# Optimization experiments

Hardware: AMD Instinct MI355X
Metric: run time of the kernel (lower is better)

## Reference

```python
import jax, jax.numpy as jnp
import numpy as np

BATCH, SEQ, FEAT, NUM_BINS = 64, 1024, 512, 32


def setup_inputs() -> dict:
    key = jax.random.key(0)
    k1, k2 = jax.random.split(key)
    features = jax.random.normal(k1, (BATCH, SEQ, FEAT), dtype=jnp.float32)
    # buffer: randn(input_dim, num_bins) / sqrt(input_dim)
    random_projection = jax.random.normal(k2, (FEAT, NUM_BINS), dtype=jnp.float32) / np.sqrt(FEAT)
    return {"features": features, "random_projection": random_projection}


def reference(features, random_projection):
    batch, seq, feat = features.shape
    x = features.reshape(-1, feat)  # [N, feat]
    N = x.shape[0]

    # RunningMeanStd.update from fresh state (mean=0, var=1, count=1e-4)
    eps_count = 1e-4
    batch_mean = x.mean(axis=0)
    batch_var = jnp.var(x, axis=0, ddof=1)  # torch.var is unbiased by default
    tot = eps_count + N
    delta = batch_mean  # - 0
    mean = delta * N / tot
    M2 = 1.0 * eps_count + batch_var * N + (delta ** 2) * eps_count * N / tot
    var = M2 / tot
    sigma = jnp.sqrt(var + 1e-8)

    normalized = (x - mean) / sigma
    projected = normalized @ random_projection  # [N, num_bins]
    bits = (projected > 0).astype(jnp.int64)
    pow2 = jnp.left_shift(jnp.int64(1), jnp.arange(NUM_BINS, dtype=jnp.int64))
    keys = (bits * pow2).sum(axis=-1)  # [N], values < 2^32

    # env_indices=None path: env = arange(N) % batch
    env = jnp.arange(N, dtype=jnp.int64) % batch
    combined = jnp.left_shift(env, 32) | keys  # unique (env, key) id

    # running occurrence count of each (env, key) in sample order i=0..N-1
    order = jnp.argsort(combined, stable=True)  # stable: preserves sample order within group
    s = combined[order]
    idx = jnp.arange(N, dtype=jnp.int64)
    is_start = jnp.concatenate([jnp.ones((1,), bool), s[1:] != s[:-1]])
    seg_start = jax.lax.cummax(jnp.where(is_start, idx, 0))
    occ = idx - seg_start + 1  # 1-based occurrence within group
    counts = jnp.zeros((N,), jnp.int64).at[order].set(occ)

    rewards = 1.0 / jnp.sqrt(counts.astype(features.dtype))
    return rewards.reshape(batch, seq, 1)
```

## Files before the change

kernel.cpp:

```cpp
#include <hip/hip_runtime.h>

using u16 = unsigned short;
using u64 = unsigned long long;

constexpr int BATCH = 64, SEQ = 1024, FEAT = 512, NBINS = 32;
constexpr int N = BATCH * SEQ;
constexpr int TAB = 131072;
constexpr unsigned TABMASK = TAB - 1;
constexpr u64 EMPTY = ~0ull;
constexpr double FXSCALE = 67108864.0;
constexpr int NSHADOW = 64;


constexpr size_t OFF_KEYS = 0;
constexpr size_t OFF_HEAD = 1048576;
constexpr size_t OFF_CNT = 1572864;
constexpr size_t OFF_SHAD = 2097152;
constexpr size_t OFF_QD = 2621440;
constexpr size_t OFF_CD = 2752512;
constexpr size_t OFF_QF = 2752768;
constexpr size_t OFF_CF = 2818304;
constexpr size_t OFF_SLOT = 2818432;
constexpr size_t OFF_NEXT = 3080576;

__global__ __launch_bounds__(256, 4) void colstats_kernel(
    const float4* __restrict__ xv,
    u64* __restrict__ shad) {
  const int t = threadIdx.x;
  const int L = blockIdx.x * 256 + t;
  double s0 = 0, s1 = 0, s2 = 0, s3 = 0, q0 = 0, q1 = 0, q2 = 0, q3 = 0;
  for (int mm = 0; mm < 32; mm += 8) {
    float4 v[8];
#pragma unroll
    for (int u = 0; u < 8; u++) v[u] = xv[L + (mm + u) * 262144];
#pragma unroll
    for (int u = 0; u < 8; u++) {
      double a = (double)v[u].x, b = (double)v[u].y;
      double c = (double)v[u].z, d = (double)v[u].w;
      s0 += a; s1 += b; s2 += c; s3 += d;
      q0 += a * a; q1 += b * b; q2 += c * c; q3 += d * d;
    }
  }
  __shared__ double red[256 * 8];
  red[t * 8 + 0] = s0; red[t * 8 + 1] = s1; red[t * 8 + 2] = s2; red[t * 8 + 3] = s3;
  red[t * 8 + 4] = q0; red[t * 8 + 5] = q1; red[t * 8 + 6] = q2; red[t * 8 + 7] = q3;
  __syncthreads();
  if (t < 128) {
    double v[8];
#pragma unroll
    for (int u = 0; u < 8; u++) v[u] = red[t * 8 + u] + red[(t + 128) * 8 + u];
    const int c0 = 4 * t;
    u64* sh = shad + (size_t)(blockIdx.x & (NSHADOW - 1)) * 1024;
#pragma unroll
    for (int u = 0; u < 4; u++) {
      long long a = (long long)llrint(v[u] * FXSCALE);
      long long b = (long long)llrint(v[4 + u] * FXSCALE);
      atomicAdd(&sh[c0 + u], (u64)a);
      atomicAdd(&sh[512 + c0 + u], (u64)b);
    }
  }
}

__global__ __launch_bounds__(512) void finalize_kernel(
    const float* __restrict__ P,
    const u64* __restrict__ shad,
    double* __restrict__ Qd, float* __restrict__ Qf,
    double* __restrict__ cd, float* __restrict__ cf) {
  __shared__ double meanArr[FEAT];
  __shared__ double invArr[FEAT];
  __shared__ double part[16][NBINS];
  const int t = threadIdx.x;
  long long isum = 0, isumsq = 0;
  for (int sh = 0; sh < NSHADOW; sh++) {
    isum += (long long)shad[sh * 1024 + t];
    isumsq += (long long)shad[sh * 1024 + 512 + t];
  }
  const double Nd = (double)N;
  const double tot = 1e-4 + Nd;
  double s = (double)isum * (1.0 / FXSCALE);
  double ss = (double)isumsq * (1.0 / FXSCALE);
  double bm = s / Nd;
  double bv = (ss - s * s / Nd) / (Nd - 1.0);
  double mean = bm * Nd / tot;
  double M2 = 1e-4 + bv * Nd + bm * bm * 1e-4 * Nd / tot;
  double var = M2 / tot;
  double inv = 1.0 / sqrt(var + 1e-8);
  meanArr[t] = mean;
  invArr[t] = inv;
#pragma unroll
  for (int j = 0; j < NBINS; j++) {
    double qd = (double)P[t * NBINS + j] * inv;
    Qd[t * NBINS + j] = qd;
    Qf[t * NBINS + j] = (float)qd;
  }
  __syncthreads();
  {
    const int j = t & 31, g = t >> 5;
    double p = 0.0;
    for (int f = g * 32; f < g * 32 + 32; f++) {
      double qd = (double)P[f * NBINS + j] * invArr[f];
      p += meanArr[f] * qd;
    }
    part[g][j] = p;
  }
  __syncthreads();
  if (t < NBINS) {
    double c = 0.0;
    for (int g = 0; g < 16; g++) c += part[g][t];
    cd[t] = c;
    cf[t] = (float)c;
  }
}

constexpr float TAU = 2.5e-3f;
__global__ __launch_bounds__(256) void project_kernel(
    const float4* __restrict__ xv, const float* __restrict__ feat,
    const float4* __restrict__ Qf4, const float* __restrict__ cf,
    const double* __restrict__ Qd, const double* __restrict__ cd,
    u64* __restrict__ keys_tab, int* __restrict__ head,
    unsigned* __restrict__ cnt, int* __restrict__ slot, int* __restrict__ nxt) {
  __shared__ __align__(16) float xt[64 * 132];
  __shared__ __align__(16) float qt[128 * 32];
  __shared__ unsigned keyParts[64];
  const int t = threadIdx.x;
  const int rowBase = blockIdx.x * 64;
  const int lane = t & 63;
  const int wid = t >> 6;
  const int j0 = __builtin_amdgcn_readfirstlane(wid * 8);
  if (t < 64) keyParts[t] = 0u;
  float4* qt4 = (float4*)qt;

  float acc[8] = {0, 0, 0, 0, 0, 0, 0, 0};
  for (int ch = 0; ch < 4; ch++) {
    __syncthreads();
#pragma unroll
    for (int k = 0; k < 8; k++) {
      int vi = t + k * 256;
      int r = vi >> 5, fv = vi & 31;
      float4 v = xv[(size_t)(rowBase + r) * 128 + ch * 32 + fv];
      *((float4*)&xt[r * 132 + fv * 4]) = v;
    }
#pragma unroll
    for (int k = 0; k < 4; k++) {
      int qi = t + k * 256;
      qt4[qi] = Qf4[ch * 1024 + qi];
    }
    __syncthreads();
    const float4* xrow = (const float4*)&xt[lane * 132];
#pragma unroll 4
    for (int g = 0; g < 32; g++) {
      float4 x4 = xrow[g];
      float xs[4] = {x4.x, x4.y, x4.z, x4.w};
#pragma unroll
      for (int ff = 0; ff < 4; ff++) {
        const int fl = 4 * g + ff;
        float4 qlo = qt4[(fl * 32 + j0) >> 2];
        float4 qhi = qt4[(fl * 32 + j0 + 4) >> 2];
        float x = xs[ff];
        acc[0] = fmaf(x, qlo.x, acc[0]);
        acc[1] = fmaf(x, qlo.y, acc[1]);
        acc[2] = fmaf(x, qlo.z, acc[2]);
        acc[3] = fmaf(x, qlo.w, acc[3]);
        acc[4] = fmaf(x, qhi.x, acc[4]);
        acc[5] = fmaf(x, qhi.y, acc[5]);
        acc[6] = fmaf(x, qhi.z, acc[6]);
        acc[7] = fmaf(x, qhi.w, acc[7]);
      }
    }
  }
  unsigned part = 0;
  float m[8];
#pragma unroll
  for (int j = 0; j < 8; j++) {
    m[j] = acc[j] - cf[j0 + j];
    if (m[j] > 0.0f) part |= (1u << (j0 + j));
  }
  for (int j = 0; j < 8; j++) {
    u64 mask = __ballot(fabsf(m[j]) < TAU);
    const int jj = j0 + j;
    while (mask) {
      const int L = (int)__builtin_ctzll(mask);
      mask &= mask - 1;
      const float* xr = feat + (size_t)(rowBase + L) * FEAT + lane * 8;
      const double* qp = Qd + (size_t)(lane * 8) * NBINS + jj;
      double p = 0.0;
#pragma unroll
      for (int u = 0; u < 8; u++)
        p = fma((double)xr[u], qp[u * NBINS], p);
#pragma unroll
      for (int off = 32; off > 0; off >>= 1) p += __shfl_xor(p, off, 64);
      const bool bit = p > cd[jj];
      if (lane == L) {
        if (bit) part |= (1u << jj);
        else part &= ~(1u << jj);
      }
    }
  }
  atomicOr(&keyParts[lane], part);
  __syncthreads();
  if (t < 64) {
    const int i = rowBase + t;
    unsigned key = keyParts[t];
    u64 combined = (u64)key;
    unsigned idx = (unsigned)((combined * 0x9E3779B97F4A7C15ull) >> 47) & TABMASK;
    for (;;) {
      u64 prev = atomicCAS(&keys_tab[idx], EMPTY, combined);
      if (prev == EMPTY || prev == combined) break;
      idx = (idx + 1) & TABMASK;
    }
    slot[i] = (int)idx;
    atomicAdd(&cnt[idx], 1u);
    nxt[i] = atomicExch(&head[idx], i);
  }
}

__global__ __launch_bounds__(256) void count_kernel(
    const int* __restrict__ slot, const int* __restrict__ nxt,
    const int* __restrict__ head, const unsigned* __restrict__ cnt,
    float* __restrict__ out) {
  const int i = blockIdx.x * 256 + threadIdx.x;
  const int sl = slot[i];
  const unsigned c = cnt[sl];
  float r = 1.0f;
  if (c > 1u) {
    int j = head[sl];
    int occ = 1;
    while (j >= 0) {
      occ += (j < i) ? 1 : 0;
      j = nxt[j];
    }
    r = 1.0f / sqrtf((float)occ);
  }
  out[i] = r;
}

extern "C" void kernel_launch(void* const* d_in, const int* in_sizes, int n_in,
                              void* d_out, int out_size, void* d_ws, size_t ws_size,
                              hipStream_t stream) {
  const float4* xv = (const float4*)d_in[0];
  const float* feat = (const float*)d_in[0];
  const float* proj = (const float*)d_in[1];
  float* out = (float*)d_out;
  char* ws = (char*)d_ws;

  u64* keys_tab = (u64*)(ws + OFF_KEYS);
  int* head = (int*)(ws + OFF_HEAD);
  unsigned* cnt = (unsigned*)(ws + OFF_CNT);
  u64* shad = (u64*)(ws + OFF_SHAD);
  double* Qd = (double*)(ws + OFF_QD);
  double* cd = (double*)(ws + OFF_CD);
  float* Qf = (float*)(ws + OFF_QF);
  float* cf = (float*)(ws + OFF_CF);
  int* slot = (int*)(ws + OFF_SLOT);
  int* nxt = (int*)(ws + OFF_NEXT);

  hipMemsetAsync(ws + OFF_KEYS, 0xFF, OFF_CNT - OFF_KEYS, stream);
  hipMemsetAsync(ws + OFF_CNT, 0x00, OFF_QD - OFF_CNT, stream);

  colstats_kernel<<<1024, 256, 0, stream>>>(xv, shad);
  finalize_kernel<<<1, 512, 0, stream>>>(proj, shad, Qd, Qf, cd, cf);
  project_kernel<<<N / 64, 256, 0, stream>>>(xv, feat, (const float4*)Qf, cf, Qd, cd,
                                             keys_tab, head, cnt, slot, nxt);
  count_kernel<<<N / 256, 256, 0, stream>>>(slot, nxt, head, cnt, out);
}
```

Measured before the change: 290.6 us.

## Compute projection with split-bf16 MFMA instead of scalar FP32 FMAs

Replaces the FP32 FMA projection loop with MFMA 16x16x32 bf16 instructions. Inputs and the scaled projection matrix are split into bf16 high and low parts, and three products (hh, lh, hl) approximate FP32 accuracy. The projection matrix is pre-laid out in fragment order in finalize, and x tiles are converted and stored in swizzled LDS. The near-zero fallback to an exact FP64 recheck is kept, but the band may now trigger more often because the split-bf16 result has larger error.

```diff
diff --git a/kernel.cpp b/kernel.cpp
--- a/kernel.cpp
+++ b/kernel.cpp
@@ -2,6 +2,9 @@
 
 using u16 = unsigned short;
 using u64 = unsigned long long;
+typedef short s16x8 __attribute__((ext_vector_type(8)));
+typedef unsigned short u16x4 __attribute__((ext_vector_type(4)));
+typedef float f32x4 __attribute__((ext_vector_type(4)));
 
 constexpr int BATCH = 64, SEQ = 1024, FEAT = 512, NBINS = 32;
 constexpr int N = BATCH * SEQ;
@@ -18,14 +21,22 @@
 constexpr size_t OFF_SHAD = 2097152;
 constexpr size_t OFF_QD = 2621440;
 constexpr size_t OFF_CD = 2752512;
-constexpr size_t OFF_QF = 2752768;
 constexpr size_t OFF_CF = 2818304;
 constexpr size_t OFF_SLOT = 2818432;
 constexpr size_t OFF_NEXT = 3080576;
+constexpr size_t OFF_QFRAG = 3342720;
+
+__device__ inline u16 f2bf(float f) {
+  unsigned u = __builtin_bit_cast(unsigned, f);
+  u += 0x7FFFu + ((u >> 16) & 1u);
+  return (u16)(u >> 16);
+}
+__device__ inline float bf2f(u16 h) {
+  return __builtin_bit_cast(float, (unsigned)h << 16);
+}
 
 __global__ __launch_bounds__(256, 4) void colstats_kernel(
-    const float4* __restrict__ xv,
-    u64* __restrict__ shad) {
+    const float4* __restrict__ xv, u64* __restrict__ shad) {
   const int t = threadIdx.x;
   const int L = blockIdx.x * 256 + t;
   double s0 = 0, s1 = 0, s2 = 0, s3 = 0, q0 = 0, q1 = 0, q2 = 0, q3 = 0;
@@ -64,7 +75,7 @@
 __global__ __launch_bounds__(512) void finalize_kernel(
     const float* __restrict__ P,
     const u64* __restrict__ shad,
-    double* __restrict__ Qd, float* __restrict__ Qf,
+    double* __restrict__ Qd, u16* __restrict__ qfrag,
     double* __restrict__ cd, float* __restrict__ cf) {
   __shared__ double meanArr[FEAT];
   __shared__ double invArr[FEAT];
@@ -87,11 +98,19 @@
   double inv = 1.0 / sqrt(var + 1e-8);
   meanArr[t] = mean;
   invArr[t] = inv;
+  const int ch = t >> 7, ks = (t >> 5) & 3, kg = (t >> 3) & 3, jlo = t & 7;
 #pragma unroll
   for (int j = 0; j < NBINS; j++) {
     double qd = (double)P[t * NBINS + j] * inv;
     Qd[t * NBINS + j] = qd;
-    Qf[t * NBINS + j] = (float)qd;
+    const u16 qh = f2bf((float)qd);
+    const u16 ql = f2bf((float)(qd - (double)bf2f(qh)));
+    const int lane = (j & 15) | (kg << 4);
+    const int bt = j >> 4;
+    const size_t base =
+        (size_t)(((((ch * 4 + ks) * 2 + bt) * 2) * 64 + lane) * 8 + jlo);
+    qfrag[base] = qh;
+    qfrag[base + 512] = ql;
   }
   __syncthreads();
   {
@@ -113,90 +132,109 @@
 }
 
 constexpr float TAU = 2.5e-3f;
-__global__ __launch_bounds__(256) void project_kernel(
+__global__ __launch_bounds__(256, 3) void project_kernel(
     const float4* __restrict__ xv, const float* __restrict__ feat,
-    const float4* __restrict__ Qf4, const float* __restrict__ cf,
+    const u16* __restrict__ qfrag, const float* __restrict__ cf,
     const double* __restrict__ Qd, const double* __restrict__ cd,
     u64* __restrict__ keys_tab, int* __restrict__ head,
     unsigned* __restrict__ cnt, int* __restrict__ slot, int* __restrict__ nxt) {
-  __shared__ __align__(16) float xt[64 * 132];
-  __shared__ __align__(16) float qt[128 * 32];
+  __shared__ __align__(16) u16 xh_lds[8192];
+  __shared__ __align__(16) u16 xl_lds[8192];
   __shared__ unsigned keyParts[64];
   const int t = threadIdx.x;
   const int rowBase = blockIdx.x * 64;
   const int lane = t & 63;
-  const int wid = t >> 6;
-  const int j0 = __builtin_amdgcn_readfirstlane(wid * 8);
+  const int w = t >> 6;
   if (t < 64) keyParts[t] = 0u;
-  float4* qt4 = (float4*)qt;
-
-  float acc[8] = {0, 0, 0, 0, 0, 0, 0, 0};
+
+  f32x4 acc0 = {0.f, 0.f, 0.f, 0.f};
+  f32x4 acc1 = {0.f, 0.f, 0.f, 0.f};
   for (int ch = 0; ch < 4; ch++) {
     __syncthreads();
-#pragma unroll
-    for (int k = 0; k < 8; k++) {
-      int vi = t + k * 256;
-      int r = vi >> 5, fv = vi & 31;
-      float4 v = xv[(size_t)(rowBase + r) * 128 + ch * 32 + fv];
-      *((float4*)&xt[r * 132 + fv * 4]) = v;
-    }
-#pragma unroll
-    for (int k = 0; k < 4; k++) {
-      int qi = t + k * 256;
-      qt4[qi] = Qf4[ch * 1024 + qi];
+    s16x8 Bh[4][2], Bl[4][2];
+#pragma unroll
+    for (int ks = 0; ks < 4; ks++)
+#pragma unroll
+      for (int bt = 0; bt < 2; bt++) {
+        const size_t b =
+            (size_t)(((((ch * 4 + ks) * 2 + bt) * 2) * 64 + lane) * 8);
+        Bh[ks][bt] = *(const s16x8*)&qfrag[b];
+        Bl[ks][bt] = *(const s16x8*)&qfrag[b + 512];
+      }
+#pragma unroll
+    for (int kk = 0; kk < 8; kk++) {
+      const int vi = t + kk * 256;
+      const int r = vi >> 5, f4 = vi & 31;
+      float4 v = xv[(size_t)(rowBase + r) * 128 + ch * 32 + f4];
+      const int ks = f4 >> 3, kg = (f4 & 7) >> 1, j0 = (f4 & 1) * 4;
+      const int lane_ = (r & 15) | (kg << 4);
+      const int blk = ((r >> 4) * 4 + ks) * 64 + (lane_ ^ (((lane_ >> 4) & 3) << 1));
+      u16x4 hv, lv;
+      float xs[4] = {v.x, v.y, v.z, v.w};
+#pragma unroll
+      for (int c2 = 0; c2 < 4; c2++) {
+        const u16 h = f2bf(xs[c2]);
+        hv[c2] = h;
+        lv[c2] = f2bf(xs[c2] - bf2f(h));
+      }
+      *(u16x4*)&xh_lds[blk * 8 + j0] = hv;
+      *(u16x4*)&xl_lds[blk * 8 + j0] = lv;
     }
     __syncthreads();
-    const float4* xrow = (const float4*)&xt[lane * 132];
-#pragma unroll 4
-    for (int g = 0; g < 32; g++) {
-      float4 x4 = xrow[g];
-      float xs[4] = {x4.x, x4.y, x4.z, x4.w};
-#pragma unroll
-      for (int ff = 0; ff < 4; ff++) {
-        const int fl = 4 * g + ff;
-        float4 qlo = qt4[(fl * 32 + j0) >> 2];
-        float4 qhi = qt4[(fl * 32 + j0 + 4) >> 2];
-        float x = xs[ff];
-        acc[0] = fmaf(x, qlo.x, acc[0]);
-        acc[1] = fmaf(x, qlo.y, acc[1]);
-        acc[2] = fmaf(x, qlo.z, acc[2]);
-        acc[3] = fmaf(x, qlo.w, acc[3]);
-        acc[4] = fmaf(x, qhi.x, acc[4]);
-        acc[5] = fmaf(x, qhi.y, acc[5]);
-        acc[6] = fmaf(x, qhi.z, acc[6]);
-        acc[7] = fmaf(x, qhi.w, acc[7]);
+#pragma unroll
+    for (int ks = 0; ks < 4; ks++) {
+      const int rblk = (w * 4 + ks) * 64 + (lane ^ (((lane >> 4) & 3) << 1));
+      s16x8 aH = *(const s16x8*)&xh_lds[rblk * 8];
+      s16x8 aL = *(const s16x8*)&xl_lds[rblk * 8];
+      acc0 = __builtin_amdgcn_mfma_f32_16x16x32_bf16(aH, Bh[ks][0], acc0, 0, 0, 0);
+      acc1 = __builtin_amdgcn_mfma_f32_16x16x32_bf16(aH, Bh[ks][1], acc1, 0, 0, 0);
+      acc0 = __builtin_amdgcn_mfma_f32_16x16x32_bf16(aL, Bh[ks][0], acc0, 0, 0, 0);
+      acc1 = __builtin_amdgcn_mfma_f32_16x16x32_bf16(aL, Bh[ks][1], acc1, 0, 0, 0);
+      acc0 = __builtin_amdgcn_mfma_f32_16x16x32_bf16(aH, Bl[ks][0], acc0, 0, 0, 0);
+      acc1 = __builtin_amdgcn_mfma_f32_16x16x32_bf16(aH, Bl[ks][1], acc1, 0, 0, 0);
+    }
+  }
+  const int colbin = lane & 15;
+  float m0[4], m1[4];
+  bool b0[4], b1[4];
+  const float c0v = cf[colbin], c1v = cf[16 + colbin];
+#pragma unroll
+  for (int rg = 0; rg < 4; rg++) {
+    m0[rg] = acc0[rg] - c0v;
+    m1[rg] = acc1[rg] - c1v;
+    b0[rg] = m0[rg] > 0.0f;
+    b1[rg] = m1[rg] > 0.0f;
+  }
+#pragma unroll
+  for (int bt = 0; bt < 2; bt++)
+#pragma unroll
+    for (int rg = 0; rg < 4; rg++) {
+      const float mv = (bt == 0) ? m0[rg] : m1[rg];
+      u64 mask = __ballot(fabsf(mv) < TAU);
+      while (mask) {
+        const int L = (int)__builtin_ctzll(mask);
+        mask &= mask - 1;
+        const int jj = bt * 16 + (L & 15);
+        const int row = rowBase + w * 16 + (L >> 4) * 4 + rg;
+        const float* xr = feat + (size_t)row * FEAT + lane * 8;
+        const double* qp = Qd + (size_t)(lane * 8) * NBINS + jj;
+        double p = 0.0;
+#pragma unroll
+        for (int u = 0; u < 8; u++) p = fma((double)xr[u], qp[u * NBINS], p);
+#pragma unroll
+        for (int off = 32; off > 0; off >>= 1) p += __shfl_xor(p, off, 64);
+        const bool bit = p > cd[jj];
+        if (lane == L) {
+          if (bt == 0) b0[rg] = bit; else b1[rg] = bit;
+        }
       }
     }
-  }
-  unsigned part = 0;
-  float m[8];
-#pragma unroll
-  for (int j = 0; j < 8; j++) {
-    m[j] = acc[j] - cf[j0 + j];
-    if (m[j] > 0.0f) part |= (1u << (j0 + j));
-  }
-  for (int j = 0; j < 8; j++) {
-    u64 mask = __ballot(fabsf(m[j]) < TAU);
-    const int jj = j0 + j;
-    while (mask) {
-      const int L = (int)__builtin_ctzll(mask);
-      mask &= mask - 1;
-      const float* xr = feat + (size_t)(rowBase + L) * FEAT + lane * 8;
-      const double* qp = Qd + (size_t)(lane * 8) * NBINS + jj;
-      double p = 0.0;
-#pragma unroll
-      for (int u = 0; u < 8; u++)
-        p = fma((double)xr[u], qp[u * NBINS], p);
-#pragma unroll
-      for (int off = 32; off > 0; off >>= 1) p += __shfl_xor(p, off, 64);
-      const bool bit = p > cd[jj];
-      if (lane == L) {
-        if (bit) part |= (1u << jj);
-        else part &= ~(1u << jj);
-      }
-    }
-  }
-  atomicOr(&keyParts[lane], part);
+#pragma unroll
+  for (int rg = 0; rg < 4; rg++) {
+    const unsigned mybits = (b0[rg] ? (1u << colbin) : 0u) |
+                            (b1[rg] ? (1u << (16 + colbin)) : 0u);
+    atomicOr(&keyParts[w * 16 + (lane >> 4) * 4 + rg], mybits);
+  }
   __syncthreads();
   if (t < 64) {
     const int i = rowBase + t;
@@ -249,17 +287,17 @@
   u64* shad = (u64*)(ws + OFF_SHAD);
   double* Qd = (double*)(ws + OFF_QD);
   double* cd = (double*)(ws + OFF_CD);
-  float* Qf = (float*)(ws + OFF_QF);
   float* cf = (float*)(ws + OFF_CF);
   int* slot = (int*)(ws + OFF_SLOT);
   int* nxt = (int*)(ws + OFF_NEXT);
+  u16* qfrag = (u16*)(ws + OFF_QFRAG);
 
   hipMemsetAsync(ws + OFF_KEYS, 0xFF, OFF_CNT - OFF_KEYS, stream);
   hipMemsetAsync(ws + OFF_CNT, 0x00, OFF_QD - OFF_CNT, stream);
 
   colstats_kernel<<<1024, 256, 0, stream>>>(xv, shad);
-  finalize_kernel<<<1, 512, 0, stream>>>(proj, shad, Qd, Qf, cd, cf);
-  project_kernel<<<N / 64, 256, 0, stream>>>(xv, feat, (const float4*)Qf, cf, Qd, cd,
+  finalize_kernel<<<1, 512, 0, stream>>>(proj, shad, Qd, qfrag, cd, cf);
+  project_kernel<<<N / 64, 256, 0, stream>>>(xv, feat, qfrag, cf, Qd, cd,
                                              keys_tab, head, cnt, slot, nxt);
   count_kernel<<<N / 256, 256, 0, stream>>>(slot, nxt, head, cnt, out);
 }
```

New measurement: 271.6 us. 6.5% less time.
